# Kernel tuning notes

Hardware: AMD Instinct MI355X
Metric: run time of the kernel (lower is better)

Reference implementation:

```python
import jax, jax.numpy as jnp
import numpy as np

B, T, H = 64, 1024, 512

def setup_inputs() -> dict:
    key = jax.random.key(0)
    ks = jax.random.split(key, 7)
    s = 1.0 / np.sqrt(H)  # torch nn.RNN/Linear init scale (uniform +-1/sqrt(H)); use normal*s for simplicity of magnitudes
    return {
        "inputs": jax.random.normal(ks[0], (B, T, 1), dtype=jnp.float32),
        "state": jnp.zeros((1, B, H), dtype=jnp.float32),
        "W_ih": jax.random.normal(ks[1], (H, 1), dtype=jnp.float32) * s,
        "W_hh": jax.random.normal(ks[2], (H, H), dtype=jnp.float32) * s,
        "b_ih": jax.random.normal(ks[3], (H,), dtype=jnp.float32) * s,
        "b_hh": jax.random.normal(ks[4], (H,), dtype=jnp.float32) * s,
        "W_out": jax.random.normal(ks[5], (1, H), dtype=jnp.float32) * s,
        "b_out": jax.random.normal(ks[6], (1,), dtype=jnp.float32) * s,
    }

def reference(inputs, state, W_ih, W_hh, b_ih, b_hh, W_out, b_out):
    # NOTE: original forward ignores the passed `state` and lets nn.RNN use a
    # zero initial hidden state; we reproduce that faithfully.
    B_, T_, _ = inputs.shape
    Hd = W_hh.shape[0]
    # precompute input projection for all timesteps: [T, B, H]
    xp = jnp.einsum('bti,hi->tbh', inputs, W_ih) + b_ih + b_hh
    h0 = jnp.zeros((B_, Hd), dtype=inputs.dtype)

    def step(h, xp_t):
        h_new = jnp.tanh(xp_t + h @ W_hh.T)
        return h_new, h_new

    h_last, Y = jax.lax.scan(step, h0, xp)  # Y: [T, B, H]
    output = h_last @ W_out.T + b_out       # [B, 1]
    new_state = h_last[None]                 # [1, B, H]
    return (output, new_state)
```

## Files before the change

### kernel.cpp

```cpp
#include <hip/hip_runtime.h>
#include <hip/hip_fp16.h>


#define BB 64
#define TT 1024
#define HH 512

typedef _Float16 half2_t __attribute__((ext_vector_type(2)));

__device__ __forceinline__ float dot2f(unsigned h, unsigned w, float acc) {
#if __has_builtin(__builtin_amdgcn_fdot2)
    return __builtin_amdgcn_fdot2(__builtin_bit_cast(half2_t, h),
                                  __builtin_bit_cast(half2_t, w), acc, false);
#else
    __half2 hh = __builtin_bit_cast(__half2, h);
    __half2 ww = __builtin_bit_cast(__half2, w);
    acc = fmaf(__low2float(hh), __low2float(ww), acc);
    return fmaf(__high2float(hh), __high2float(ww), acc);
#endif
}

__device__ __forceinline__ float fast_tanh(float z) {
    float e = __expf(2.0f * z);
    return fmaf(-2.0f, __builtin_amdgcn_rcpf(e + 1.0f), 1.0f);
}

__launch_bounds__(256, 1)
__global__ void rnn_persist(const float* __restrict__ x,
                            const float* __restrict__ W_ih,
                            const float* __restrict__ W_hh,
                            const float* __restrict__ b_ih,
                            const float* __restrict__ b_hh,
                            const float* __restrict__ W_out,
                            const float* __restrict__ b_out,
                            float* __restrict__ out,
                            unsigned long long* __restrict__ hg)
{
    const int q    = blockIdx.x >> 6;
    const int b    = blockIdx.x & 63;
    const int tid  = threadIdx.x;
    const int w    = tid >> 6;
    const int lane = tid & 63;

    __shared__ float parts[2][4][128];
    __shared__ float xrow[TT];
    __shared__ __align__(16) unsigned h2w[4][64];

    for (int i = tid; i < TT; i += 256) xrow[i] = x[b * TT + i];

    const int j0 = q * 128 + lane;
    const int j1 = j0 + 64;
    const int k0 = w * 128;
    unsigned wh0[64], wh1[64];
    {
        const float2* r0 = reinterpret_cast<const float2*>(W_hh + (size_t)j0 * HH + k0);
        const float2* r1 = reinterpret_cast<const float2*>(W_hh + (size_t)j1 * HH + k0);
#pragma unroll
        for (int d = 0; d < 64; ++d) {
            float2 a = r0[d], c = r1[d];
            wh0[d] = __builtin_bit_cast(unsigned, __floats2half2_rn(a.x, a.y));
            wh1[d] = __builtin_bit_cast(unsigned, __floats2half2_rn(c.x, c.y));
        }
    }

    const int s_slot = 16 * w + lane;
    float wihA = 0.f, wihB = 0.f, bA = 0.f, bB = 0.f;
    if (lane < 16) {
        const int ja = q * 128 + 2 * s_slot, jb = ja + 1;
        wihA = W_ih[ja]; wihB = W_ih[jb];
        bA = b_ih[ja] + b_hh[ja];
        bB = b_ih[jb] + b_hh[jb];
    }

#pragma unroll 1
    for (int t = 0; t < TT; ++t) {
        float a0 = 0.f, a1 = 0.f;
        if (t > 0) {
            const unsigned long long* pp =
                &hg[(((size_t)(t & 1) * BB + b) * 4 + w) * 64 + lane];
            unsigned long long v =
                __hip_atomic_load(pp, __ATOMIC_RELAXED, __HIP_MEMORY_SCOPE_AGENT);
            while ((unsigned)(v >> 32) != (unsigned)t) {
                __builtin_amdgcn_s_sleep(1);
                v = __hip_atomic_load(pp, __ATOMIC_RELAXED, __HIP_MEMORY_SCOPE_AGENT);
            }
            h2w[w][lane] = (unsigned)v;

            const uint4* hp = reinterpret_cast<const uint4*>(&h2w[w][0]);
#pragma unroll
            for (int c = 0; c < 16; ++c) {
                const uint4 u = hp[c];
                a0 = dot2f(u.x, wh0[4*c+0], a0); a1 = dot2f(u.x, wh1[4*c+0], a1);
                a0 = dot2f(u.y, wh0[4*c+1], a0); a1 = dot2f(u.y, wh1[4*c+1], a1);
                a0 = dot2f(u.z, wh0[4*c+2], a0); a1 = dot2f(u.z, wh1[4*c+2], a1);
                a0 = dot2f(u.w, wh0[4*c+3], a0); a1 = dot2f(u.w, wh1[4*c+3], a1);
            }
        }
        parts[t & 1][w][lane]      = a0;
        parts[t & 1][w][lane + 64] = a1;
        __syncthreads();

        if (lane < 16) {
            const float* pb = &parts[t & 1][0][0];
            const float2 p0 = *reinterpret_cast<const float2*>(pb + 0 * 128 + 2 * s_slot);
            const float2 p1 = *reinterpret_cast<const float2*>(pb + 1 * 128 + 2 * s_slot);
            const float2 p2 = *reinterpret_cast<const float2*>(pb + 2 * 128 + 2 * s_slot);
            const float2 p3 = *reinterpret_cast<const float2*>(pb + 3 * 128 + 2 * s_slot);
            float zA = (p0.x + p1.x) + (p2.x + p3.x);
            float zB = (p0.y + p1.y) + (p2.y + p3.y);
            const float xt = xrow[t];
            zA = fmaf(xt, wihA, zA + bA);
            zB = fmaf(xt, wihB, zB + bB);
            const float hA = fast_tanh(zA);
            const float hB = fast_tanh(zB);
            const unsigned d = __builtin_bit_cast(unsigned, __floats2half2_rn(hA, hB));
            const unsigned long long pv =
                ((unsigned long long)(unsigned)(t + 1) << 32) | d;
            __hip_atomic_store(
                &hg[(((size_t)((t + 1) & 1) * BB + b) * 4 + q) * 64 + s_slot], pv,
                __ATOMIC_RELAXED, __HIP_MEMORY_SCOPE_AGENT);
            if (t == TT - 1) {
                out[64 + b * HH + q * 128 + 2 * s_slot]     = hA;
                out[64 + b * HH + q * 128 + 2 * s_slot + 1] = hB;
            }
        }
    }

    if (q == 0 && w == 0) {
        float s = 0.f;
#pragma unroll
        for (int sl = 0; sl < 4; ++sl) {
            const unsigned long long* pp =
                &hg[(((size_t)(TT & 1) * BB + b) * 4 + sl) * 64 + lane];
            unsigned long long v =
                __hip_atomic_load(pp, __ATOMIC_RELAXED, __HIP_MEMORY_SCOPE_AGENT);
            while ((unsigned)(v >> 32) != (unsigned)TT) {
                __builtin_amdgcn_s_sleep(1);
                v = __hip_atomic_load(pp, __ATOMIC_RELAXED, __HIP_MEMORY_SCOPE_AGENT);
            }
            const __half2 hh = __builtin_bit_cast(__half2, (unsigned)v);
            s = fmaf(__low2float(hh),  W_out[sl * 128 + 2 * lane],     s);
            s = fmaf(__high2float(hh), W_out[sl * 128 + 2 * lane + 1], s);
        }
#pragma unroll
        for (int off = 32; off; off >>= 1) s += __shfl_down(s, off, 64);
        if (lane == 0) out[b] = s + b_out[0];
    }
}

extern "C" void kernel_launch(void* const* d_in, const int* in_sizes, int n_in,
                              void* d_out, int out_size, void* d_ws, size_t ws_size,
                              hipStream_t stream) {
    const float* x     = (const float*)d_in[0];
    const float* W_ih  = (const float*)d_in[2];
    const float* W_hh  = (const float*)d_in[3];
    const float* b_ih  = (const float*)d_in[4];
    const float* b_hh  = (const float*)d_in[5];
    const float* W_out = (const float*)d_in[6];
    const float* b_out = (const float*)d_in[7];

    unsigned long long* hg = (unsigned long long*)d_ws;

    hipMemsetAsync(hg, 0, 2ull * BB * 4 * 64 * sizeof(unsigned long long), stream);

    rnn_persist<<<dim3(256), dim3(256), 0, stream>>>(
        x, W_ih, W_hh, b_ih, b_hh, W_out, b_out, (float*)d_out, hg);
}
```

Measured before the change: 1.279 ms.

## Run each batch row's recurrence in one workgroup instead of cross-block flag sync

Each batch row's full recurrence now runs inside one 512-thread workgroup, replacing the four cooperating blocks per row that exchanged hidden state through global-memory atomic flags and spin-waits. The full 512x512 fp16 W_hh slice is held per block, three quarters in registers and one quarter in LDS with an XOR swizzle. The step-to-step handoff becomes a shared-memory buffer plus __syncthreads, which removes global polling latency and the workspace memset. The cost is only 64 blocks, each doing four times the dot-product work per step, plus heavy register and LDS pressure that may cause spills.

Measured after the change: 1.467 ms. 1.15x slower.

```diff
diff --git a/kernel.cpp b/kernel.cpp
--- a/kernel.cpp
+++ b/kernel.cpp
@@ -5,6 +5,8 @@
 #define BB 64
 #define TT 1024
 #define HH 512
+#define REG_CH 24
+#define LDS_CH 8
 
 typedef _Float16 half2_t __attribute__((ext_vector_type(2)));
 
@@ -25,123 +27,126 @@
     return fmaf(-2.0f, __builtin_amdgcn_rcpf(e + 1.0f), 1.0f);
 }
 
-__launch_bounds__(256, 1)
-__global__ void rnn_persist(const float* __restrict__ x,
-                            const float* __restrict__ W_ih,
-                            const float* __restrict__ W_hh,
-                            const float* __restrict__ b_ih,
-                            const float* __restrict__ b_hh,
-                            const float* __restrict__ W_out,
-                            const float* __restrict__ b_out,
-                            float* __restrict__ out,
-                            unsigned long long* __restrict__ hg)
+__device__ __forceinline__ unsigned pack_h2(float a, float b) {
+    return __builtin_bit_cast(unsigned, __floats2half2_rn(a, b));
+}
+
+__launch_bounds__(512, 2)
+__global__ void rnn_batch_cu(const float* __restrict__ x,
+                             const float* __restrict__ W_ih,
+                             const float* __restrict__ W_hh,
+                             const float* __restrict__ b_ih,
+                             const float* __restrict__ b_hh,
+                             const float* __restrict__ W_out,
+                             const float* __restrict__ b_out,
+                             float* __restrict__ out)
 {
-    const int q    = blockIdx.x >> 6;
-    const int b    = blockIdx.x & 63;
+    const int b    = blockIdx.x;
     const int tid  = threadIdx.x;
     const int w    = tid >> 6;
     const int lane = tid & 63;
+    const int i    = lane & 31;
+    const int c    = lane >> 5;
 
-    __shared__ float parts[2][4][128];
+    __shared__ unsigned h2[2][HH / 2];
     __shared__ float xrow[TT];
-    __shared__ __align__(16) unsigned h2w[4][64];
+    __shared__ __align__(16) unsigned wtail[512 * 64];
 
-    for (int i = tid; i < TT; i += 256) xrow[i] = x[b * TT + i];
+    const int jA    = 64 * w + 2 * i;
+    const int jB    = jA + 1;
+    const int kbase = c * 256;
 
-    const int j0 = q * 128 + lane;
-    const int j1 = j0 + 64;
-    const int k0 = w * 128;
-    unsigned wh0[64], wh1[64];
+    for (int s = tid; s < TT; s += 512) xrow[s] = x[b * TT + s];
+
+    unsigned wrA[96], wrB[96];
     {
-        const float2* r0 = reinterpret_cast<const float2*>(W_hh + (size_t)j0 * HH + k0);
-        const float2* r1 = reinterpret_cast<const float2*>(W_hh + (size_t)j1 * HH + k0);
+        const float2* rA = reinterpret_cast<const float2*>(W_hh + (size_t)jA * HH + kbase);
+        const float2* rB = reinterpret_cast<const float2*>(W_hh + (size_t)jB * HH + kbase);
 #pragma unroll
-        for (int d = 0; d < 64; ++d) {
-            float2 a = r0[d], c = r1[d];
-            wh0[d] = __builtin_bit_cast(unsigned, __floats2half2_rn(a.x, a.y));
-            wh1[d] = __builtin_bit_cast(unsigned, __floats2half2_rn(c.x, c.y));
+        for (int d = 0; d < 96; ++d) {
+            float2 a = rA[d], e = rB[d];
+            wrA[d] = pack_h2(a.x, a.y);
+            wrB[d] = pack_h2(e.x, e.y);
+        }
+        uint4* tb = reinterpret_cast<uint4*>(&wtail[tid * 64]);
+#pragma unroll
+        for (int l = 0; l < 16; ++l) {
+            const float2* rr = (l < 8) ? rA : rB;
+            const int d0 = 96 + 4 * (l & 7);
+            float2 p0 = rr[d0], p1 = rr[d0 + 1], p2 = rr[d0 + 2], p3 = rr[d0 + 3];
+            uint4 u;
+            u.x = pack_h2(p0.x, p0.y);
+            u.y = pack_h2(p1.x, p1.y);
+            u.z = pack_h2(p2.x, p2.y);
+            u.w = pack_h2(p3.x, p3.y);
+            tb[(l & 8) | ((l ^ tid) & 7)] = u;
         }
     }
 
-    const int s_slot = 16 * w + lane;
-    float wihA = 0.f, wihB = 0.f, bA = 0.f, bB = 0.f;
-    if (lane < 16) {
-        const int ja = q * 128 + 2 * s_slot, jb = ja + 1;
-        wihA = W_ih[ja]; wihB = W_ih[jb];
-        bA = b_ih[ja] + b_hh[ja];
-        bB = b_ih[jb] + b_hh[jb];
-    }
+    const float wihA = W_ih[jA], wihB = W_ih[jB];
+    const float bA = b_ih[jA] + b_hh[jA];
+    const float bB = b_ih[jB] + b_hh[jB];
+
+    __syncthreads();
 
 #pragma unroll 1
     for (int t = 0; t < TT; ++t) {
-        float a0 = 0.f, a1 = 0.f;
+        float aA0 = 0.f, aA1 = 0.f, aB0 = 0.f, aB1 = 0.f;
         if (t > 0) {
-            const unsigned long long* pp =
-                &hg[(((size_t)(t & 1) * BB + b) * 4 + w) * 64 + lane];
-            unsigned long long v =
-                __hip_atomic_load(pp, __ATOMIC_RELAXED, __HIP_MEMORY_SCOPE_AGENT);
-            while ((unsigned)(v >> 32) != (unsigned)t) {
-                __builtin_amdgcn_s_sleep(1);
-                v = __hip_atomic_load(pp, __ATOMIC_RELAXED, __HIP_MEMORY_SCOPE_AGENT);
+            const uint4* hp = reinterpret_cast<const uint4*>(&h2[t & 1][c * 128]);
+            const uint4* tb = reinterpret_cast<const uint4*>(&wtail[tid * 64]);
+#pragma unroll
+            for (int ch = 0; ch < REG_CH; ++ch) {
+                const uint4 u = hp[ch];
+                aA0 = dot2f(u.x, wrA[4*ch+0], aA0); aB0 = dot2f(u.x, wrB[4*ch+0], aB0);
+                aA1 = dot2f(u.y, wrA[4*ch+1], aA1); aB1 = dot2f(u.y, wrB[4*ch+1], aB1);
+                aA0 = dot2f(u.z, wrA[4*ch+2], aA0); aB0 = dot2f(u.z, wrB[4*ch+2], aB0);
+                aA1 = dot2f(u.w, wrA[4*ch+3], aA1); aB1 = dot2f(u.w, wrB[4*ch+3], aB1);
             }
-            h2w[w][lane] = (unsigned)v;
-
-            const uint4* hp = reinterpret_cast<const uint4*>(&h2w[w][0]);
 #pragma unroll
-            for (int c = 0; c < 16; ++c) {
-                const uint4 u = hp[c];
-                a0 = dot2f(u.x, wh0[4*c+0], a0); a1 = dot2f(u.x, wh1[4*c+0], a1);
-                a0 = dot2f(u.y, wh0[4*c+1], a0); a1 = dot2f(u.y, wh1[4*c+1], a1);
-                a0 = dot2f(u.z, wh0[4*c+2], a0); a1 = dot2f(u.z, wh1[4*c+2], a1);
-                a0 = dot2f(u.w, wh0[4*c+3], a0); a1 = dot2f(u.w, wh1[4*c+3], a1);
+            for (int ch = 0; ch < LDS_CH; ++ch) {
+                const uint4 u  = hp[REG_CH + ch];
+                const uint4 wa = tb[(ch ^ tid) & 7];
+                const uint4 wb = tb[8 | ((ch ^ tid) & 7)];
+                aA0 = dot2f(u.x, wa.x, aA0); aB0 = dot2f(u.x, wb.x, aB0);
+                aA1 = dot2f(u.y, wa.y, aA1); aB1 = dot2f(u.y, wb.y, aB1);
+                aA0 = dot2f(u.z, wa.z, aA0); aB0 = dot2f(u.z, wb.z, aB0);
+                aA1 = dot2f(u.w, wa.w, aA1); aB1 = dot2f(u.w, wb.w, aB1);
             }
         }
-        parts[t & 1][w][lane]      = a0;
-        parts[t & 1][w][lane + 64] = a1;
-        __syncthreads();
-
-        if (lane < 16) {
-            const float* pb = &parts[t & 1][0][0];
-            const float2 p0 = *reinterpret_cast<const float2*>(pb + 0 * 128 + 2 * s_slot);
-            const float2 p1 = *reinterpret_cast<const float2*>(pb + 1 * 128 + 2 * s_slot);
-            const float2 p2 = *reinterpret_cast<const float2*>(pb + 2 * 128 + 2 * s_slot);
-            const float2 p3 = *reinterpret_cast<const float2*>(pb + 3 * 128 + 2 * s_slot);
-            float zA = (p0.x + p1.x) + (p2.x + p3.x);
-            float zB = (p0.y + p1.y) + (p2.y + p3.y);
-            const float xt = xrow[t];
-            zA = fmaf(xt, wihA, zA + bA);
-            zB = fmaf(xt, wihB, zB + bB);
-            const float hA = fast_tanh(zA);
-            const float hB = fast_tanh(zB);
-            const unsigned d = __builtin_bit_cast(unsigned, __floats2half2_rn(hA, hB));
-            const unsigned long long pv =
-                ((unsigned long long)(unsigned)(t + 1) << 32) | d;
-            __hip_atomic_store(
-                &hg[(((size_t)((t + 1) & 1) * BB + b) * 4 + q) * 64 + s_slot], pv,
-                __ATOMIC_RELAXED, __HIP_MEMORY_SCOPE_AGENT);
+        float zA = aA0 + aA1;
+        float zB = aB0 + aB1;
+        zA += __shfl_xor(zA, 32, 64);
+        zB += __shfl_xor(zB, 32, 64);
+        const float xt = xrow[t];
+        zA = fmaf(xt, wihA, zA + bA);
+        zB = fmaf(xt, wihB, zB + bB);
+        const float hA = fast_tanh(zA);
+        const float hB = fast_tanh(zB);
+        if (c == 0) {
+            h2[(t + 1) & 1][32 * w + i] = pack_h2(hA, hB);
             if (t == TT - 1) {
-                out[64 + b * HH + q * 128 + 2 * s_slot]     = hA;
-                out[64 + b * HH + q * 128 + 2 * s_slot + 1] = hB;
+                out[64 + b * HH + jA] = hA;
+                out[64 + b * HH + jB] = hB;
             }
         }
+        __syncthreads();
     }
 
-    if (q == 0 && w == 0) {
+    if (w == 0) {
+        const uint4 hv = reinterpret_cast<const uint4*>(&h2[TT & 1][0])[lane];
+        const float4 w0 = reinterpret_cast<const float4*>(W_out)[2 * lane + 0];
+        const float4 w1 = reinterpret_cast<const float4*>(W_out)[2 * lane + 1];
         float s = 0.f;
-#pragma unroll
-        for (int sl = 0; sl < 4; ++sl) {
-            const unsigned long long* pp =
-                &hg[(((size_t)(TT & 1) * BB + b) * 4 + sl) * 64 + lane];
-            unsigned long long v =
-                __hip_atomic_load(pp, __ATOMIC_RELAXED, __HIP_MEMORY_SCOPE_AGENT);
-            while ((unsigned)(v >> 32) != (unsigned)TT) {
-                __builtin_amdgcn_s_sleep(1);
-                v = __hip_atomic_load(pp, __ATOMIC_RELAXED, __HIP_MEMORY_SCOPE_AGENT);
-            }
-            const __half2 hh = __builtin_bit_cast(__half2, (unsigned)v);
-            s = fmaf(__low2float(hh),  W_out[sl * 128 + 2 * lane],     s);
-            s = fmaf(__high2float(hh), W_out[sl * 128 + 2 * lane + 1], s);
-        }
+        __half2 p;
+        p = __builtin_bit_cast(__half2, hv.x);
+        s = fmaf(__low2float(p), w0.x, s); s = fmaf(__high2float(p), w0.y, s);
+        p = __builtin_bit_cast(__half2, hv.y);
+        s = fmaf(__low2float(p), w0.z, s); s = fmaf(__high2float(p), w0.w, s);
+        p = __builtin_bit_cast(__half2, hv.z);
+        s = fmaf(__low2float(p), w1.x, s); s = fmaf(__high2float(p), w1.y, s);
+        p = __builtin_bit_cast(__half2, hv.w);
+        s = fmaf(__low2float(p), w1.z, s); s = fmaf(__high2float(p), w1.w, s);
 #pragma unroll
         for (int off = 32; off; off >>= 1) s += __shfl_down(s, off, 64);
         if (lane == 0) out[b] = s + b_out[0];
@@ -159,10 +164,6 @@
     const float* W_out = (const float*)d_in[6];
     const float* b_out = (const float*)d_in[7];
 
-    unsigned long long* hg = (unsigned long long*)d_ws;
-
-    hipMemsetAsync(hg, 0, 2ull * BB * 4 * 64 * sizeof(unsigned long long), stream);
-
-    rnn_persist<<<dim3(256), dim3(256), 0, stream>>>(
-        x, W_ih, W_hh, b_ih, b_hh, W_out, b_out, (float*)d_out, hg);
+    rnn_batch_cu<<<dim3(BB), dim3(512), 0, stream>>>(
+        x, W_ih, W_hh, b_ih, b_hh, W_out, b_out, (float*)d_out);
 }
```

## Co-locate each batch's four blocks on one XCD via dynamic team assignment

Applied to the files above, without the earlier changes.

Launches 512 blocks and has each one read its XCD id. An atomic counter per XCD groups blocks into teams of four on the same XCD, and each team claims one batch row; blocks left without a row exit. The four blocks exchanging the hidden state for a batch therefore share one L2, so cross-block polling should not have to cross XCDs. Polling now uses an inline L2-coherent atomic-add-zero read with plain dwordx2 stores, the block's own hidden slice is reused from LDS without a global poll, and the tail is computed by a full wavefront instead of 16 lanes. The change relies on enough blocks landing on each XCD and on inline asm cache semantics, and a team that never fills could hang or leave batch rows missing.

New measurement: 1.426 ms. +11.5%, slower.

```diff
diff --git a/kernel.cpp b/kernel.cpp
--- a/kernel.cpp
+++ b/kernel.cpp
@@ -25,19 +25,37 @@
     return fmaf(-2.0f, __builtin_amdgcn_rcpf(e + 1.0f), 1.0f);
 }
 
-__launch_bounds__(256, 1)
-__global__ void rnn_persist(const float* __restrict__ x,
-                            const float* __restrict__ W_ih,
-                            const float* __restrict__ W_hh,
-                            const float* __restrict__ b_ih,
-                            const float* __restrict__ b_hh,
-                            const float* __restrict__ W_out,
-                            const float* __restrict__ b_out,
-                            float* __restrict__ out,
-                            unsigned long long* __restrict__ hg)
+__device__ __forceinline__ unsigned pack_h2(float a, float b) {
+    return __builtin_bit_cast(unsigned, __floats2half2_rn(a, b));
+}
+
+__device__ __forceinline__ unsigned long long l2_read_u64(unsigned long long* p) {
+    unsigned long long old;
+    unsigned long long zero = 0;
+    asm volatile("global_atomic_add_x2 %0, %1, %2, off sc0\n\t"
+                 "s_waitcnt vmcnt(0)"
+                 : "=v"(old) : "v"(p), "v"(zero) : "memory");
+    return old;
+}
+
+__device__ __forceinline__ void l2_write_u64(unsigned long long* p, unsigned long long v) {
+    asm volatile("global_store_dwordx2 %0, %1, off" :: "v"(p), "v"(v) : "memory");
+}
+
+#define AG __HIP_MEMORY_SCOPE_AGENT
+
+__launch_bounds__(256, 2)
+__global__ void rnn_xcd(const float* __restrict__ x,
+                        const float* __restrict__ W_ih,
+                        const float* __restrict__ W_hh,
+                        const float* __restrict__ b_ih,
+                        const float* __restrict__ b_hh,
+                        const float* __restrict__ W_out,
+                        const float* __restrict__ b_out,
+                        float* __restrict__ out,
+                        unsigned* __restrict__ ctl,
+                        unsigned long long* __restrict__ hg)
 {
-    const int q    = blockIdx.x >> 6;
-    const int b    = blockIdx.x & 63;
     const int tid  = threadIdx.x;
     const int w    = tid >> 6;
     const int lane = tid & 63;
@@ -45,8 +63,41 @@
     __shared__ float parts[2][4][128];
     __shared__ float xrow[TT];
     __shared__ __align__(16) unsigned h2w[4][64];
-
-    for (int i = tid; i < TT; i += 256) xrow[i] = x[b * TT + i];
+    __shared__ __align__(16) unsigned h2local[2][64];
+    __shared__ unsigned shr;
+
+    if (tid == 0) {
+        unsigned xcd;
+        asm volatile("s_getreg_b32 %0, hwreg(HW_REG_XCC_ID)" : "=s"(xcd));
+        xcd &= 7;
+        unsigned slot = __hip_atomic_fetch_add(&ctl[2 + xcd], 1u, __ATOMIC_RELAXED, AG);
+        unsigned team = slot >> 2, role = slot & 3;
+        unsigned* tb = &ctl[16 + xcd * 128 + team];
+        unsigned enc;
+        if (role == 3) {
+            unsigned bt = __hip_atomic_fetch_add(&ctl[0], 1u, __ATOMIC_RELAXED, AG);
+            enc = (bt < BB) ? (0x100u | bt) : 0x1FFu;
+            __hip_atomic_store(tb, enc, __ATOMIC_RELEASE, AG);
+            if (bt < BB) __hip_atomic_fetch_add(&ctl[1], 1u, __ATOMIC_RELEASE, AG);
+        } else {
+            for (;;) {
+                enc = __hip_atomic_load(tb, __ATOMIC_ACQUIRE, AG);
+                if (enc) break;
+                if (__hip_atomic_load(&ctl[1], __ATOMIC_ACQUIRE, AG) >= BB) {
+                    enc = __hip_atomic_load(tb, __ATOMIC_ACQUIRE, AG);
+                    if (!enc) enc = 0x1FFu;
+                    break;
+                }
+                __builtin_amdgcn_s_sleep(8);
+            }
+        }
+        shr = enc | (role << 16);
+    }
+    __syncthreads();
+    const unsigned er = shr;
+    if ((er & 0xFFu) == 0xFFu) return;
+    const int b = er & 0xFFu;
+    const int q = (er >> 16) & 3;
 
     const int j0 = q * 128 + lane;
     const int j1 = j0 + 64;
@@ -58,35 +109,43 @@
 #pragma unroll
         for (int d = 0; d < 64; ++d) {
             float2 a = r0[d], c = r1[d];
-            wh0[d] = __builtin_bit_cast(unsigned, __floats2half2_rn(a.x, a.y));
-            wh1[d] = __builtin_bit_cast(unsigned, __floats2half2_rn(c.x, c.y));
-        }
-    }
-
-    const int s_slot = 16 * w + lane;
-    float wihA = 0.f, wihB = 0.f, bA = 0.f, bB = 0.f;
-    if (lane < 16) {
-        const int ja = q * 128 + 2 * s_slot, jb = ja + 1;
-        wihA = W_ih[ja]; wihB = W_ih[jb];
-        bA = b_ih[ja] + b_hh[ja];
-        bB = b_ih[jb] + b_hh[jb];
-    }
+            wh0[d] = pack_h2(a.x, a.y);
+            wh1[d] = pack_h2(c.x, c.y);
+        }
+    }
+    for (int s = tid; s < TT; s += 256) xrow[s] = x[b * TT + s];
+
+    const int jA = q * 128 + 2 * lane, jB = jA + 1;
+    const float wihA = W_ih[jA], wihB = W_ih[jB];
+    const float bA = b_ih[jA] + b_hh[jA];
+    const float bB = b_ih[jB] + b_hh[jB];
+
+    unsigned long long* pollp[2];
+    unsigned long long* pubp[2];
+#pragma unroll
+    for (int p = 0; p < 2; ++p) {
+        pollp[p] = hg + (((size_t)p * BB + b) * 4 + w) * 64 + lane;
+        pubp[p]  = hg + (((size_t)p * BB + b) * 4 + q) * 64 + lane;
+    }
+
+    __syncthreads();
 
 #pragma unroll 1
     for (int t = 0; t < TT; ++t) {
+        const int par = t & 1;
         float a0 = 0.f, a1 = 0.f;
         if (t > 0) {
-            const unsigned long long* pp =
-                &hg[(((size_t)(t & 1) * BB + b) * 4 + w) * 64 + lane];
-            unsigned long long v =
-                __hip_atomic_load(pp, __ATOMIC_RELAXED, __HIP_MEMORY_SCOPE_AGENT);
-            while ((unsigned)(v >> 32) != (unsigned)t) {
-                __builtin_amdgcn_s_sleep(1);
-                v = __hip_atomic_load(pp, __ATOMIC_RELAXED, __HIP_MEMORY_SCOPE_AGENT);
-            }
-            h2w[w][lane] = (unsigned)v;
-
-            const uint4* hp = reinterpret_cast<const uint4*>(&h2w[w][0]);
+            const unsigned* hsrc;
+            if (w != q) {
+                unsigned long long v = l2_read_u64(pollp[par]);
+                while ((unsigned)(v >> 32) != (unsigned)t)
+                    v = l2_read_u64(pollp[par]);
+                h2w[w][lane] = (unsigned)v;
+                hsrc = &h2w[w][0];
+            } else {
+                hsrc = &h2local[par][0];
+            }
+            const uint4* hp = reinterpret_cast<const uint4*>(hsrc);
 #pragma unroll
             for (int c = 0; c < 16; ++c) {
                 const uint4 u = hp[c];
@@ -96,16 +155,17 @@
                 a0 = dot2f(u.w, wh0[4*c+3], a0); a1 = dot2f(u.w, wh1[4*c+3], a1);
             }
         }
-        parts[t & 1][w][lane]      = a0;
-        parts[t & 1][w][lane + 64] = a1;
+        parts[par][w][lane]      = a0;
+        parts[par][w][lane + 64] = a1;
         __syncthreads();
 
-        if (lane < 16) {
-            const float* pb = &parts[t & 1][0][0];
-            const float2 p0 = *reinterpret_cast<const float2*>(pb + 0 * 128 + 2 * s_slot);
-            const float2 p1 = *reinterpret_cast<const float2*>(pb + 1 * 128 + 2 * s_slot);
-            const float2 p2 = *reinterpret_cast<const float2*>(pb + 2 * 128 + 2 * s_slot);
-            const float2 p3 = *reinterpret_cast<const float2*>(pb + 3 * 128 + 2 * s_slot);
+        if (w == q) {
+            const int s2 = 2 * lane;
+            const float* pb = &parts[par][0][0];
+            const float2 p0 = *reinterpret_cast<const float2*>(pb + 0 * 128 + s2);
+            const float2 p1 = *reinterpret_cast<const float2*>(pb + 1 * 128 + s2);
+            const float2 p2 = *reinterpret_cast<const float2*>(pb + 2 * 128 + s2);
+            const float2 p3 = *reinterpret_cast<const float2*>(pb + 3 * 128 + s2);
             float zA = (p0.x + p1.x) + (p2.x + p3.x);
             float zB = (p0.y + p1.y) + (p2.y + p3.y);
             const float xt = xrow[t];
@@ -113,31 +173,31 @@
             zB = fmaf(xt, wihB, zB + bB);
             const float hA = fast_tanh(zA);
             const float hB = fast_tanh(zB);
-            const unsigned d = __builtin_bit_cast(unsigned, __floats2half2_rn(hA, hB));
-            const unsigned long long pv =
-                ((unsigned long long)(unsigned)(t + 1) << 32) | d;
-            __hip_atomic_store(
-                &hg[(((size_t)((t + 1) & 1) * BB + b) * 4 + q) * 64 + s_slot], pv,
-                __ATOMIC_RELAXED, __HIP_MEMORY_SCOPE_AGENT);
+            const unsigned du = pack_h2(hA, hB);
+            const unsigned long long wv =
+                ((unsigned long long)(unsigned)(t + 1) << 32) | du;
+            l2_write_u64(pubp[par ^ 1], wv);
+            h2local[par ^ 1][lane] = du;
             if (t == TT - 1) {
-                out[64 + b * HH + q * 128 + 2 * s_slot]     = hA;
-                out[64 + b * HH + q * 128 + 2 * s_slot + 1] = hB;
+                out[64 + b * HH + jA] = hA;
+                out[64 + b * HH + jB] = hB;
             }
         }
     }
 
     if (q == 0 && w == 0) {
         float s = 0.f;
-#pragma unroll
-        for (int sl = 0; sl < 4; ++sl) {
-            const unsigned long long* pp =
-                &hg[(((size_t)(TT & 1) * BB + b) * 4 + sl) * 64 + lane];
-            unsigned long long v =
-                __hip_atomic_load(pp, __ATOMIC_RELAXED, __HIP_MEMORY_SCOPE_AGENT);
-            while ((unsigned)(v >> 32) != (unsigned)TT) {
-                __builtin_amdgcn_s_sleep(1);
-                v = __hip_atomic_load(pp, __ATOMIC_RELAXED, __HIP_MEMORY_SCOPE_AGENT);
-            }
+        {
+            const __half2 hh = __builtin_bit_cast(__half2, h2local[TT & 1][lane]);
+            s = fmaf(__low2float(hh),  W_out[2 * lane],     s);
+            s = fmaf(__high2float(hh), W_out[2 * lane + 1], s);
+        }
+#pragma unroll
+        for (int sl = 1; sl < 4; ++sl) {
+            unsigned long long* p =
+                hg + (((size_t)(TT & 1) * BB + b) * 4 + sl) * 64 + lane;
+            unsigned long long v = l2_read_u64(p);
+            while ((unsigned)(v >> 32) != (unsigned)TT) v = l2_read_u64(p);
             const __half2 hh = __builtin_bit_cast(__half2, (unsigned)v);
             s = fmaf(__low2float(hh),  W_out[sl * 128 + 2 * lane],     s);
             s = fmaf(__high2float(hh), W_out[sl * 128 + 2 * lane + 1], s);
@@ -159,10 +219,11 @@
     const float* W_out = (const float*)d_in[6];
     const float* b_out = (const float*)d_in[7];
 
-    unsigned long long* hg = (unsigned long long*)d_ws;
-
-    hipMemsetAsync(hg, 0, 2ull * BB * 4 * 64 * sizeof(unsigned long long), stream);
-
-    rnn_persist<<<dim3(256), dim3(256), 0, stream>>>(
-        x, W_ih, W_hh, b_ih, b_hh, W_out, b_out, (float*)d_out, hg);
-}
+    unsigned* ctl = (unsigned*)d_ws;
+    unsigned long long* hg = (unsigned long long*)((char*)d_ws + 8192);
+
+    hipMemsetAsync(d_ws, 0, 8192 + 2ull * BB * 4 * 64 * 8, stream);
+
+    rnn_xcd<<<dim3(512), dim3(256), 0, stream>>>(
+        x, W_ih, W_hh, b_ih, b_hh, W_out, b_out, (float*)d_out, ctl, hg);
+}
```
